# Performance work log

Measured on AMD Instinct MI355X. Metric: run time of the kernel, lower is better.

## Reference

```python
import jax, jax.numpy as jnp
import numpy as np


def setup_inputs() -> dict:
    key = jax.random.key(0)
    ks = jax.random.split(key, 7)
    B = 32768
    x = jax.random.normal(ks[0], (B, 1, 28, 28), dtype=jnp.float32)
    # learned params (AtomicLinear weight/bias per layer)
    w1 = jax.random.normal(ks[1], (128, 784), dtype=jnp.float32)
    b1 = jax.random.normal(ks[2], (128,), dtype=jnp.float32)
    w2 = jax.random.normal(ks[3], (256, 128), dtype=jnp.float32)
    b2 = jax.random.normal(ks[4], (256,), dtype=jnp.float32)
    w3 = jax.random.normal(ks[5], (10, 256), dtype=jnp.float32)
    b3 = jax.random.normal(ks[6], (10,), dtype=jnp.float32)
    return {"x": x, "w1": w1, "b1": b1, "w2": w2, "b2": b2, "w3": w3, "b3": b3}


def reference(x, w1, b1, w2, b2, w3, b3):
    # AtomicLinear: (x[:,None,:] * W) gathered by a random permutation over
    # in_features, then summed over that axis. Summation is permutation-
    # invariant, so this is exactly x @ W.T + b.
    B = x.shape[0]
    h = x.reshape(B, -1)                      # [B, 784]
    h = jax.nn.relu(h @ w1.T + b1)            # [B, 128]
    h = jax.nn.relu(h @ w2.T + b2)            # [B, 256]
    logits = h @ w3.T + b3                    # [B, 10]
    return jax.nn.log_softmax(logits, axis=1)
```

## Files before the change

### kernel.cpp

```cpp
#include <hip/hip_runtime.h>
#include <hip/hip_bf16.h>
#include <math.h>


#define TPB 512

#define W2K 106496
#define W3K 139264
#define NCHUNK_TOT 17920

typedef __attribute__((ext_vector_type(8))) short bf16x8;
typedef __attribute__((ext_vector_type(4))) float f32x4;

static __device__ inline short f2bf(float f) {
    union { float f; unsigned u; } v; v.f = f;
    unsigned r = v.u + 0x7fffu + ((v.u >> 16) & 1u);
    return (short)(r >> 16);
}
static __device__ inline bf16x8 cvt8(float4 a, float4 b) {
    union { __hip_bfloat162 h2[4]; bf16x8 v; } u;
    u.h2[0] = __float22bfloat162_rn(make_float2(a.x, a.y));
    u.h2[1] = __float22bfloat162_rn(make_float2(a.z, a.w));
    u.h2[2] = __float22bfloat162_rn(make_float2(b.x, b.y));
    u.h2[3] = __float22bfloat162_rn(make_float2(b.z, b.w));
    return u.v;
}
static __device__ inline void gld16(const void* g, void* l) {
    __builtin_amdgcn_global_load_lds(
        (const __attribute__((address_space(1))) unsigned int*)g,
        (__attribute__((address_space(3))) unsigned int*)l, 16, 0, 0);
}

__global__ void prep_pack(const float* __restrict__ w1,
                          const float* __restrict__ w2,
                          const float* __restrict__ w3,
                          short* __restrict__ wb) {
    const int tid = blockIdx.x * blockDim.x + threadIdx.x;
    if (tid >= NCHUNK_TOT) return;
    float4 a = make_float4(0,0,0,0), b = a;
    size_t dst;
    if (tid < 13312) {
        const int kt = tid >> 10, rem = tid & 1023, row = rem >> 3, phys = rem & 7;
        const int kg = kt * 64 + ((phys ^ (row & 7)) << 3);
        if (kg + 8 <= 784) {
            const float* p = &w1[(size_t)row * 784 + kg];
            a = *(const float4*)p; b = *(const float4*)(p + 4);
        }
        dst = (size_t)tid * 8;
    } else if (tid < 17408) {
        const int t2 = tid - 13312;
        const int kt = t2 >> 10, rem = t2 & 1023, row = rem >> 2, phys = rem & 3;
        const int kg = kt * 32 + ((phys ^ (row & 3)) << 3);
        const float* p = &w2[(size_t)row * 128 + kg];
        a = *(const float4*)p; b = *(const float4*)(p + 4);
        dst = (size_t)W2K + (size_t)t2 * 8;
    } else {
        const int t3 = tid - 17408;
        const int row = t3 >> 5, phys = t3 & 31;
        const int kg = (phys ^ (row & 7)) << 3;
        if (row < 10) {
            const float* p = &w3[(size_t)row * 256 + kg];
            a = *(const float4*)p; b = *(const float4*)(p + 4);
        }
        dst = (size_t)W3K + (size_t)t3 * 8;
    }
    *(bf16x8*)&wb[dst] = cvt8(a, b);
}

__global__ __launch_bounds__(TPB, 4) void mnist_v9(
    const float* __restrict__ x,
    const float* __restrict__ b1v,
    const float* __restrict__ b2v,
    const float* __restrict__ b3v,
    const short* __restrict__ wb,
    float* __restrict__ out)
{
    __shared__ __align__(16) char smem[80 * 1024];
    float* const xb  = (float*)smem;
    short* const wbf = (short*)(smem + 32 * 1024);
    short* const h1  = (short*)(smem + 64 * 1024);
    short* const w2l = (short*)smem;
    short* const h2  = wbf;
    short* const w3l = h1;

    const int t    = threadIdx.x;
    const int lane = t & 63;
    const int wv   = t >> 6;
    const int mi   = wv >> 1;
    const int nh   = wv & 1;
    const int l15  = lane & 15;
    const int l4   = lane >> 4;
    const int row0 = blockIdx.x * 64;

    const size_t XLAST = (size_t)32768 * 3136 - 16;

    auto stage_x = [&](int kt, float* dst) {
        #pragma unroll
        for (int p = 0; p < 2; ++p) {
            const int rloc = wv * 8 + p * 4;
            const int rl   = rloc + (lane >> 4);
            const int logs = (lane & 15) ^ (rl & 15);
            size_t off = (size_t)(row0 + rl) * 3136 + (size_t)kt * 256
                       + (size_t)logs * 16;
            if (off > XLAST) off = XLAST;
            gld16((const char*)x + off, dst + rloc * 64);
        }
    };
    auto stage_w1 = [&](int kt, short* dst) {
        #pragma unroll
        for (int p = 0; p < 2; ++p) {
            const int rloc = wv * 16 + p * 8;
            gld16(wb + (size_t)kt * 8192 + rloc * 64 + lane * 8, dst + rloc * 64);
        }
    };
    auto stage_w2 = [&](int kt, short* dst) {
        #pragma unroll
        for (int p = 0; p < 2; ++p) {
            const int rloc = wv * 32 + p * 16;
            gld16(wb + W2K + (size_t)kt * 8192 + rloc * 32 + lane * 8, dst + rloc * 32);
        }
    };

    stage_x(0, xb);
    stage_w1(0, wbf);
    __syncthreads();

    f32x4 acc1[4];
    #pragma unroll
    for (int nf = 0; nf < 4; ++nf) acc1[nf] = (f32x4){0.f,0.f,0.f,0.f};

    const int arow = 16 * mi + l15;
    for (int kt = 0; kt < 13; ++kt) {
        const int cur = kt & 1;
        if (kt < 12) {
            stage_x(kt + 1, xb + (cur ^ 1) * 4096);
            stage_w1(kt + 1, wbf + (cur ^ 1) * 8192);
        }
        const float* xt = xb + cur * 4096;
        const short* wt = wbf + cur * 8192;
        #pragma unroll
        for (int kk = 0; kk < 2; ++kk) {
            const int s0 = kk * 8 + l4 * 2;
            const float4 fa = *(const float4*)&xt[arow * 64 + ((s0 ^ l15) << 2)];
            const float4 fb = *(const float4*)&xt[arow * 64 + (((s0 + 1) ^ l15) << 2)];
            const bf16x8 a = cvt8(fa, fb);
            #pragma unroll
            for (int nf = 0; nf < 4; ++nf) {
                const int rB = nh * 64 + nf * 16 + l15;
                const int phys = (kk * 4 + l4) ^ (rB & 7);
                const bf16x8 b = *(const bf16x8*)&wt[rB * 64 + phys * 8];
                acc1[nf] = __builtin_amdgcn_mfma_f32_16x16x32_bf16(a, b, acc1[nf], 0, 0, 0);
            }
        }
        __syncthreads();
    }

    stage_w2(0, w2l);
    stage_w2(1, w2l + 8192);
    #pragma unroll
    for (int nf = 0; nf < 4; ++nf) {
        const int c = nh * 64 + nf * 16 + l15;
        const float bc = b1v[c];
        #pragma unroll
        for (int i = 0; i < 4; ++i) {
            const int r = mi * 16 + l4 * 4 + i;
            const float h = fmaxf(acc1[nf][i] + bc, 0.f);
            h1[r * 128 + (((c >> 3) ^ (r & 7)) << 3) + (c & 7)] = f2bf(h);
        }
    }
    __syncthreads();

    bf16x8 a2[4];
    {
        #pragma unroll
        for (int kk = 0; kk < 4; ++kk)
            a2[kk] = *(const bf16x8*)&h1[arow * 128 + (((kk * 4 + l4) ^ (arow & 7)) << 3)];
    }
    __syncthreads();

    {
        const int rloc = wv * 2;
        gld16(wb + W3K + rloc * 256 + lane * 8, w3l + rloc * 256);
    }

    f32x4 acc2[8];
    #pragma unroll
    for (int nf = 0; nf < 8; ++nf) acc2[nf] = (f32x4){0.f,0.f,0.f,0.f};

    #pragma unroll
    for (int kt = 0; kt < 4; ++kt) {
        const short* wt2 = w2l + (kt & 1) * 8192;
        #pragma unroll
        for (int nf = 0; nf < 8; ++nf) {
            const int rB = nh * 128 + nf * 16 + l15;
            const int phys = l4 ^ (rB & 3);
            const bf16x8 b = *(const bf16x8*)&wt2[rB * 32 + phys * 8];
            acc2[nf] = __builtin_amdgcn_mfma_f32_16x16x32_bf16(a2[kt], b, acc2[nf], 0, 0, 0);
        }
        __syncthreads();
        if (kt < 2)
            stage_w2(kt + 2, w2l + (kt & 1) * 8192);
    }

    #pragma unroll
    for (int nf = 0; nf < 8; ++nf) {
        const int c = nh * 128 + nf * 16 + l15;
        const float bc = b2v[c];
        #pragma unroll
        for (int i = 0; i < 4; ++i) {
            const int r = mi * 16 + l4 * 4 + i;
            const float h = fmaxf(acc2[nf][i] + bc, 0.f);
            h2[r * 256 + (((c >> 3) ^ (r & 7)) << 3) + (c & 7)] = f2bf(h);
        }
    }
    __syncthreads();

    if (nh == 0) {
        f32x4 acc3 = (f32x4){0.f,0.f,0.f,0.f};
        #pragma unroll
        for (int kt = 0; kt < 8; ++kt) {
            const int slot = kt * 4 + l4;
            const bf16x8 a3  = *(const bf16x8*)&h2[arow * 256 + ((slot ^ (arow & 7)) << 3)];
            const bf16x8 b3r = *(const bf16x8*)&w3l[l15 * 256 + ((slot ^ (l15 & 7)) << 3)];
            acc3 = __builtin_amdgcn_mfma_f32_16x16x32_bf16(a3, b3r, acc3, 0, 0, 0);
        }
        const float b3c = (l15 < 10) ? b3v[l15] : 0.f;
        #pragma unroll
        for (int i = 0; i < 4; ++i) {
            const float v = acc3[i] + b3c;
            float m = (l15 < 10) ? v : -1e30f;
            #pragma unroll
            for (int off = 8; off; off >>= 1) m = fmaxf(m, __shfl_xor(m, off, 16));
            const float e = (l15 < 10) ? expf(v - m) : 0.f;
            float sum = e;
            #pragma unroll
            for (int off = 8; off; off >>= 1) sum += __shfl_xor(sum, off, 16);
            const float ls = m + logf(sum);
            if (l15 < 10) {
                const int r = row0 + mi * 16 + l4 * 4 + i;
                out[(size_t)r * 10 + l15] = v - ls;
            }
        }
    }
}

extern "C" void kernel_launch(void* const* d_in, const int* in_sizes, int n_in,
                              void* d_out, int out_size, void* d_ws, size_t ws_size,
                              hipStream_t stream) {
    const float* x  = (const float*)d_in[0];
    const float* w1 = (const float*)d_in[1];
    const float* b1 = (const float*)d_in[2];
    const float* w2 = (const float*)d_in[3];
    const float* b2 = (const float*)d_in[4];
    const float* w3 = (const float*)d_in[5];
    const float* b3 = (const float*)d_in[6];
    float* out = (float*)d_out;
    short* wb  = (short*)d_ws;

    prep_pack<<<(NCHUNK_TOT + 255) / 256, 256, 0, stream>>>(w1, w2, w3, wb);

    dim3 grid(32768 / 64), block(TPB);
    mnist_v9<<<grid, block, 0, stream>>>(x, b1, b2, b3, wb, out);
}
```

Before: 33.43 us.

## Load x directly to registers and triple-buffer weight tiles with partial waits

Each lane now loads its layer-1 activation fragment straight from global memory into registers, one tile ahead, so x no longer goes through shared memory. Weight tiles move to a three-buffer rotation with prefetch distance two, and the W2 tiles are staged during the last layer-1 iterations. The full __syncthreads is replaced by s_waitcnt vmcnt plus s_barrier, so loads stay in flight across iterations and shared memory drops from 80KB to 64KB. The direct x loads are uncoalesced 16-byte reads per lane, and the hand-counted vmcnt values must match the real number of outstanding loads or the kernel reads stale data.

```diff
diff --git a/kernel.cpp b/kernel.cpp
--- a/kernel.cpp
+++ b/kernel.cpp
@@ -67,7 +67,7 @@
     *(bf16x8*)&wb[dst] = cvt8(a, b);
 }
 
-__global__ __launch_bounds__(TPB, 4) void mnist_v9(
+__global__ __launch_bounds__(TPB, 4) void mnist_v10(
     const float* __restrict__ x,
     const float* __restrict__ b1v,
     const float* __restrict__ b2v,
@@ -75,12 +75,12 @@
     const short* __restrict__ wb,
     float* __restrict__ out)
 {
-    __shared__ __align__(16) char smem[80 * 1024];
-    float* const xb  = (float*)smem;
-    short* const wbf = (short*)(smem + 32 * 1024);
-    short* const h1  = (short*)(smem + 64 * 1024);
-    short* const w2l = (short*)smem;
-    short* const h2  = wbf;
+    __shared__ __align__(16) char smem[64 * 1024];
+    short* const B0  = (short*)smem;
+    short* const B1  = B0 + 8192;
+    short* const B2  = B1 + 8192;
+    short* const h1  = B2 + 8192;
+    short* const h2  = B0;
     short* const w3l = h1;
 
     const int t    = threadIdx.x;
@@ -91,20 +91,15 @@
     const int l15  = lane & 15;
     const int l4   = lane >> 4;
     const int row0 = blockIdx.x * 64;
-
-    const size_t XLAST = (size_t)32768 * 3136 - 16;
-
-    auto stage_x = [&](int kt, float* dst) {
-        #pragma unroll
-        for (int p = 0; p < 2; ++p) {
-            const int rloc = wv * 8 + p * 4;
-            const int rl   = rloc + (lane >> 4);
-            const int logs = (lane & 15) ^ (rl & 15);
-            size_t off = (size_t)(row0 + rl) * 3136 + (size_t)kt * 256
-                       + (size_t)logs * 16;
-            if (off > XLAST) off = XLAST;
-            gld16((const char*)x + off, dst + rloc * 64);
-        }
+    const int arow = 16 * mi + l15;
+
+    const size_t XMAX  = (size_t)32768 * 3136 - 16;
+    const size_t xbase = (size_t)(row0 + arow) * 3136;
+
+    auto xld = [&](int kf) -> float4 {
+        size_t off = xbase + (size_t)kf * 4;
+        off = off > XMAX ? XMAX : off;
+        return *(const float4*)((const char*)x + off);
     };
     auto stage_w1 = [&](int kt, short* dst) {
         #pragma unroll
@@ -121,42 +116,50 @@
         }
     };
 
-    stage_x(0, xb);
-    stage_w1(0, wbf);
-    __syncthreads();
+    short *b0 = B0, *b1 = B1, *b2 = B2;
+
+    stage_w1(0, b0);
+    float4 xc0 = xld(l4 * 8),      xc1 = xld(l4 * 8 + 4);
+    float4 xc2 = xld(32 + l4 * 8), xc3 = xld(32 + l4 * 8 + 4);
+    stage_w1(1, b1);
+    asm volatile("s_waitcnt vmcnt(6)" ::: "memory");
+    __builtin_amdgcn_s_barrier();
+    __builtin_amdgcn_sched_barrier(0);
 
     f32x4 acc1[4];
     #pragma unroll
     for (int nf = 0; nf < 4; ++nf) acc1[nf] = (f32x4){0.f,0.f,0.f,0.f};
 
-    const int arow = 16 * mi + l15;
     for (int kt = 0; kt < 13; ++kt) {
-        const int cur = kt & 1;
+        float4 xn0, xn1, xn2, xn3;
         if (kt < 12) {
-            stage_x(kt + 1, xb + (cur ^ 1) * 4096);
-            stage_w1(kt + 1, wbf + (cur ^ 1) * 8192);
-        }
-        const float* xt = xb + cur * 4096;
-        const short* wt = wbf + cur * 8192;
-        #pragma unroll
-        for (int kk = 0; kk < 2; ++kk) {
-            const int s0 = kk * 8 + l4 * 2;
-            const float4 fa = *(const float4*)&xt[arow * 64 + ((s0 ^ l15) << 2)];
-            const float4 fb = *(const float4*)&xt[arow * 64 + (((s0 + 1) ^ l15) << 2)];
-            const bf16x8 a = cvt8(fa, fb);
-            #pragma unroll
-            for (int nf = 0; nf < 4; ++nf) {
-                const int rB = nh * 64 + nf * 16 + l15;
-                const int phys = (kk * 4 + l4) ^ (rB & 7);
-                const bf16x8 b = *(const bf16x8*)&wt[rB * 64 + phys * 8];
-                acc1[nf] = __builtin_amdgcn_mfma_f32_16x16x32_bf16(a, b, acc1[nf], 0, 0, 0);
-            }
-        }
-        __syncthreads();
-    }
-
-    stage_w2(0, w2l);
-    stage_w2(1, w2l + 8192);
+            const int kb = (kt + 1) * 64 + l4 * 8;
+            xn0 = xld(kb);      xn1 = xld(kb + 4);
+            xn2 = xld(kb + 32); xn3 = xld(kb + 36);
+        }
+        if (kt < 11)      stage_w1(kt + 2, b2);
+        else if (kt == 11) stage_w2(0, b2);
+        else               stage_w2(1, b2);
+
+        const bf16x8 a0 = cvt8(xc0, xc1);
+        const bf16x8 a1 = cvt8(xc2, xc3);
+        #pragma unroll
+        for (int nf = 0; nf < 4; ++nf) {
+            const int rB = nh * 64 + nf * 16 + l15;
+            const bf16x8 w0 = *(const bf16x8*)&b0[rB * 64 + ((l4 ^ (rB & 7)) << 3)];
+            const bf16x8 w1f = *(const bf16x8*)&b0[rB * 64 + (((4 + l4) ^ (rB & 7)) << 3)];
+            acc1[nf] = __builtin_amdgcn_mfma_f32_16x16x32_bf16(a0, w0, acc1[nf], 0, 0, 0);
+            acc1[nf] = __builtin_amdgcn_mfma_f32_16x16x32_bf16(a1, w1f, acc1[nf], 0, 0, 0);
+        }
+        if (kt < 12) {
+            asm volatile("s_waitcnt vmcnt(6)" ::: "memory");
+            __builtin_amdgcn_s_barrier();
+            __builtin_amdgcn_sched_barrier(0);
+            xc0 = xn0; xc1 = xn1; xc2 = xn2; xc3 = xn3;
+        }
+        short* tmp = b0; b0 = b1; b1 = b2; b2 = tmp;
+    }
+
     #pragma unroll
     for (int nf = 0; nf < 4; ++nf) {
         const int c = nh * 64 + nf * 16 + l15;
@@ -171,11 +174,9 @@
     __syncthreads();
 
     bf16x8 a2[4];
-    {
-        #pragma unroll
-        for (int kk = 0; kk < 4; ++kk)
-            a2[kk] = *(const bf16x8*)&h1[arow * 128 + (((kk * 4 + l4) ^ (arow & 7)) << 3)];
-    }
+    #pragma unroll
+    for (int kk = 0; kk < 4; ++kk)
+        a2[kk] = *(const bf16x8*)&h1[arow * 128 + (((kk * 4 + l4) ^ (arow & 7)) << 3)];
     __syncthreads();
 
     {
@@ -188,19 +189,23 @@
     for (int nf = 0; nf < 8; ++nf) acc2[nf] = (f32x4){0.f,0.f,0.f,0.f};
 
     #pragma unroll
-    for (int kt = 0; kt < 4; ++kt) {
-        const short* wt2 = w2l + (kt & 1) * 8192;
+    for (int kt2 = 0; kt2 < 4; ++kt2) {
+        if (kt2 < 2) stage_w2(kt2 + 2, b2);
         #pragma unroll
         for (int nf = 0; nf < 8; ++nf) {
             const int rB = nh * 128 + nf * 16 + l15;
-            const int phys = l4 ^ (rB & 3);
-            const bf16x8 b = *(const bf16x8*)&wt2[rB * 32 + phys * 8];
-            acc2[nf] = __builtin_amdgcn_mfma_f32_16x16x32_bf16(a2[kt], b, acc2[nf], 0, 0, 0);
-        }
-        __syncthreads();
-        if (kt < 2)
-            stage_w2(kt + 2, w2l + (kt & 1) * 8192);
-    }
+            const bf16x8 b = *(const bf16x8*)&b0[rB * 32 + ((l4 ^ (rB & 3)) << 3)];
+            acc2[nf] = __builtin_amdgcn_mfma_f32_16x16x32_bf16(a2[kt2], b, acc2[nf], 0, 0, 0);
+        }
+        if (kt2 < 3) {
+            if (kt2 == 2) asm volatile("s_waitcnt vmcnt(0)" ::: "memory");
+            else          asm volatile("s_waitcnt vmcnt(2)" ::: "memory");
+            __builtin_amdgcn_s_barrier();
+            __builtin_amdgcn_sched_barrier(0);
+        }
+        short* tmp = b0; b0 = b1; b1 = b2; b2 = tmp;
+    }
+    __syncthreads();
 
     #pragma unroll
     for (int nf = 0; nf < 8; ++nf) {
@@ -260,5 +265,5 @@
     prep_pack<<<(NCHUNK_TOT + 255) / 256, 256, 0, stream>>>(w1, w2, w3, wb);
 
     dim3 grid(32768 / 64), block(TPB);
-    mnist_v9<<<grid, block, 0, stream>>>(x, b1, b2, b3, wb, out);
-}
+    mnist_v10<<<grid, block, 0, stream>>>(x, b1, b2, b3, wb, out);
+}
```

Measured after the change: 39.77 us. 19.0% more time.
